# Optimization experiments

Measured on AMD Instinct MI355X. Metric: run time of the kernel, lower is better.

Reference implementation:

```python
import jax, jax.numpy as jnp
import numpy as np

B, C, N, K, COUT = 8, 128, 10000, 16, 256


def setup_inputs() -> dict:
    key = jax.random.key(0)
    ks = jax.random.split(key, 8)
    x = jax.random.normal(ks[0], (B, C, N, 1), dtype=jnp.float32)
    edge_index = jax.random.randint(ks[1], (2, B, N, K), 0, N)
    s1 = 1.0 / np.sqrt(C)
    W1 = jax.random.uniform(ks[2], (C, C), jnp.float32, -s1, s1)   # nn1 1x1 conv weight
    b1 = jax.random.uniform(ks[3], (C,), jnp.float32, -s1, s1)
    Wp = jax.random.uniform(ks[4], (C, C), jnp.float32, -s1, s1)   # nn_pooling Linear
    bp = jax.random.uniform(ks[5], (C,), jnp.float32, -s1, s1)
    s2 = 1.0 / np.sqrt(2 * C)
    W2 = jax.random.uniform(ks[6], (COUT, 2 * C), jnp.float32, -s2, s2)  # nn2 1x1 conv
    b2 = jax.random.uniform(ks[7], (COUT,), jnp.float32, -s2, s2)
    return dict(x=x, edge_index=edge_index, W1=W1, b1=b1, Wp=Wp, bp=bp, W2=W2, b2=b2)


def reference(x, edge_index, W1, b1, Wp, bp, W2, b2):
    b, c, n, _ = x.shape
    k = edge_index.shape[-1]
    # nn1: 1x1 conv (channel mix) + ReLU -> [B,C,N,1]
    h = jax.nn.relu(jnp.einsum('bcns,dc->bdns', x, W1) + b1[None, :, None, None])
    # batched_index_select: gather neighbor features along vertex dim -> [B,C,N,K]
    hn = h[:, :, :, 0]                              # [B,C,N]
    idx = edge_index[0].reshape(b, 1, n * k)        # broadcast over C
    xj = jnp.take_along_axis(hn, idx, axis=2).reshape(b, c, n, k)
    # nn_pooling: Linear over channel dim + ReLU (transpose(1,3) in torch == act on C)
    xj = jax.nn.relu(jnp.einsum('bcnk,dc->bdnk', xj, Wp) + bp[None, :, None, None])
    # max-pool over neighbors, keepdim -> [B,C,N,1]
    xj = jnp.max(xj, axis=-1, keepdims=True)
    # concat along channels, nn2: 1x1 conv + ReLU -> [B,COUT,N,1]
    cat = jnp.concatenate([h, xj], axis=1)
    out = jax.nn.relu(jnp.einsum('bcns,dc->bdns', cat, W2) + b2[None, :, None, None])
    return out
```

## Files before the change

kernel.cpp:

```cpp
#include <hip/hip_runtime.h>

#define NODES 10000
#define BATCH 8
#define CH    128
#define KNB   16
#define CO    256

typedef __bf16 bf16x8 __attribute__((ext_vector_type(8)));
typedef float  f32x4  __attribute__((ext_vector_type(4)));

__device__ __forceinline__ unsigned short f2bf(float f) {
  unsigned u = __float_as_uint(f);
  u = (u + 0x7FFFu + ((u >> 16) & 1u)) >> 16;
  return (unsigned short)u;
}

__device__ __forceinline__ unsigned pkmax(unsigned a, unsigned b) {
  unsigned d;
  asm("v_pk_max_u16 %0, %1, %2" : "=v"(d) : "v"(a), "v"(b));
  return d;
}
__device__ __forceinline__ uint4 pkmax4(uint4 a, uint4 b) {
  a.x = pkmax(a.x, b.x); a.y = pkmax(a.y, b.y);
  a.z = pkmax(a.z, b.z); a.w = pkmax(a.w, b.w);
  return a;
}
__device__ __forceinline__ bf16x8 asbf8(uint4 u) {
  union { uint4 u; bf16x8 b; } c; c.u = u; return c.b;
}

__global__ __launch_bounds__(256) void prep(
    const float* __restrict__ W1, const float* __restrict__ Wp,
    const float* __restrict__ W2,
    unsigned short* __restrict__ W1b, unsigned short* __restrict__ Wpb,
    unsigned short* __restrict__ W2b)
{
  int i = blockIdx.x * 256 + threadIdx.x;
  const float* src; unsigned short* dst; int off;
  if (i < 4096)      { src = W1; dst = W1b; off = i; }
  else if (i < 8192) { src = Wp; dst = Wpb; off = i - 4096; }
  else               { src = W2; dst = W2b; off = i - 8192; }
  float4 v = ((const float4*)src)[off];
  ushort4 o;
  o.x = f2bf(v.x); o.y = f2bf(v.y); o.z = f2bf(v.z); o.w = f2bf(v.w);
  ((ushort4*)dst)[off] = o;
}

__global__ __launch_bounds__(256) void fused_hz(
    const unsigned short* __restrict__ W1b, const float* __restrict__ b1,
    const unsigned short* __restrict__ Wpb, const float* __restrict__ bp,
    const float* __restrict__ x,
    unsigned short* __restrict__ h_t, unsigned short* __restrict__ z_t)
{
  const int b  = blockIdx.y;
  const int n0 = blockIdx.x * 64;
  const int t  = threadIdx.x;
  const int lane = t & 63, w = t >> 6;
  const int lm = lane & 15, q = lane >> 4;

  __shared__ __align__(16) unsigned short Bt[64 * 128];
  __shared__ __align__(16) unsigned short Ht[64 * 128];
  char* BtB = (char*)Bt;
  char* HtB = (char*)Ht;

  {
    const float* X = x + (size_t)b * CH * NODES;
#pragma unroll
    for (int rep = 0; rep < 4; ++rep) {
      int flat = t + rep * 256;
      int c2 = flat >> 4, n4 = flat & 15;
      int c  = c2 * 2;
      int gn = n0 + n4 * 4;
      float4 a0 = make_float4(0.f,0.f,0.f,0.f), a1 = a0;
      if (gn < NODES) {
        a0 = *(const float4*)(X + (size_t)c * NODES + gn);
        a1 = *(const float4*)(X + (size_t)(c + 1) * NODES + gn);
      }
      float v0[4] = {a0.x, a0.y, a0.z, a0.w};
      float v1[4] = {a1.x, a1.y, a1.z, a1.w};
#pragma unroll
      for (int i = 0; i < 4; ++i) {
        int nn = n4 * 4 + i;
        unsigned pk = (unsigned)f2bf(v0[i]) | ((unsigned)f2bf(v1[i]) << 16);
        int phys = nn * 256 + (((c2 >> 2) ^ (nn & 7)) << 4) + ((c2 & 3) << 2);
        *(unsigned*)(BtB + phys) = pk;
      }
    }
  }

  const int d0  = (w & 1) * 64;
  const int nbw = (w >> 1) * 32;

  uint4 af[4][4];
#pragma unroll
  for (int dt = 0; dt < 4; ++dt)
#pragma unroll
    for (int kt = 0; kt < 4; ++kt)
      af[dt][kt] = *(const uint4*)(W1b + (d0 + dt*16 + lm) * CH + kt*32 + q*8);

  __syncthreads();

  f32x4 acc[4][2];
#pragma unroll
  for (int dt = 0; dt < 4; ++dt)
#pragma unroll
    for (int nt = 0; nt < 2; ++nt) acc[dt][nt] = (f32x4){0.f,0.f,0.f,0.f};

#pragma unroll
  for (int kt = 0; kt < 4; ++kt)
#pragma unroll
    for (int nt = 0; nt < 2; ++nt) {
      int nl = nbw + nt * 16 + lm;
      int chunk = kt * 4 + q;
      int phys = nl * 256 + ((chunk ^ (nl & 7)) << 4);
      bf16x8 bb = asbf8(*(const uint4*)(BtB + phys));
#pragma unroll
      for (int dt = 0; dt < 4; ++dt)
        acc[dt][nt] = __builtin_amdgcn_mfma_f32_16x16x32_bf16(
            asbf8(af[dt][kt]), bb, acc[dt][nt], 0, 0, 0);
    }

  uint4 af2[4][4];
#pragma unroll
  for (int dt = 0; dt < 4; ++dt)
#pragma unroll
    for (int kt = 0; kt < 4; ++kt)
      af2[dt][kt] = *(const uint4*)(Wpb + (d0 + dt*16 + lm) * CH + kt*32 + q*8);

#pragma unroll
  for (int dt = 0; dt < 4; ++dt) {
    int dbase = d0 + dt * 16 + q * 4;
    float4 bi = *(const float4*)(b1 + dbase);
    float bv[4] = {bi.x, bi.y, bi.z, bi.w};
#pragma unroll
    for (int nt = 0; nt < 2; ++nt) {
      int nl = nbw + nt * 16 + lm;
      int gn = n0 + nl;
      ushort4 o;
      o.x = f2bf(fmaxf(acc[dt][nt][0] + bv[0], 0.f));
      o.y = f2bf(fmaxf(acc[dt][nt][1] + bv[1], 0.f));
      o.z = f2bf(fmaxf(acc[dt][nt][2] + bv[2], 0.f));
      o.w = f2bf(fmaxf(acc[dt][nt][3] + bv[3], 0.f));
      int chunk = dbase >> 3;
      int phys  = nl * 256 + ((chunk ^ (nl & 7)) << 4) + ((q & 1) << 3);
      *(ushort4*)(HtB + phys) = o;
      if (gn < NODES)
        *(ushort4*)(h_t + ((size_t)b * NODES + gn) * CH + dbase) = o;
    }
  }

  __syncthreads();

#pragma unroll
  for (int dt = 0; dt < 4; ++dt)
#pragma unroll
    for (int nt = 0; nt < 2; ++nt) acc[dt][nt] = (f32x4){0.f,0.f,0.f,0.f};

#pragma unroll
  for (int kt = 0; kt < 4; ++kt)
#pragma unroll
    for (int nt = 0; nt < 2; ++nt) {
      int nl = nbw + nt * 16 + lm;
      int chunk = kt * 4 + q;
      int phys = nl * 256 + ((chunk ^ (nl & 7)) << 4);
      bf16x8 bb = asbf8(*(const uint4*)(HtB + phys));
#pragma unroll
      for (int dt = 0; dt < 4; ++dt)
        acc[dt][nt] = __builtin_amdgcn_mfma_f32_16x16x32_bf16(
            asbf8(af2[dt][kt]), bb, acc[dt][nt], 0, 0, 0);
    }

#pragma unroll
  for (int dt = 0; dt < 4; ++dt) {
    int dbase = d0 + dt * 16 + q * 4;
    float4 bi = *(const float4*)(bp + dbase);
    float bv[4] = {bi.x, bi.y, bi.z, bi.w};
#pragma unroll
    for (int nt = 0; nt < 2; ++nt) {
      int gn = n0 + nbw + nt * 16 + lm;
      if (gn < NODES) {
        ushort4 o;
        o.x = f2bf(fmaxf(acc[dt][nt][0] + bv[0], 0.f));
        o.y = f2bf(fmaxf(acc[dt][nt][1] + bv[1], 0.f));
        o.z = f2bf(fmaxf(acc[dt][nt][2] + bv[2], 0.f));
        o.w = f2bf(fmaxf(acc[dt][nt][3] + bv[3], 0.f));
        *(ushort4*)(z_t + ((size_t)b * NODES + gn) * CH + dbase) = o;
      }
    }
  }
}

__global__ __launch_bounds__(256) void gmax_kernel(
    const unsigned short* __restrict__ z_t, const int* __restrict__ e0,
    unsigned short* __restrict__ zm)
{
  const int bid = blockIdx.x;
  const int b   = bid & 7;
  const int n0  = (bid >> 3) * 64;
  const int t   = threadIdx.x;
  const int nl  = t >> 2, c = t & 3;
  const int gn  = n0 + nl;
  if (gn >= NODES) return;

  const int* ip = e0 + ((size_t)b * NODES + gn) * KNB;
  int4 iv0 = *(const int4*)(ip);
  int4 iv1 = *(const int4*)(ip + 4);
  int4 iv2 = *(const int4*)(ip + 8);
  int4 iv3 = *(const int4*)(ip + 12);
  int idx[16] = {iv0.x, iv0.y, iv0.z, iv0.w,
                 iv1.x, iv1.y, iv1.z, iv1.w,
                 iv2.x, iv2.y, iv2.z, iv2.w,
                 iv3.x, iv3.y, iv3.z, iv3.w};

  const char* Z = (const char*)(z_t + (size_t)b * NODES * CH) + c * 16;
  uint4 m[4];
#pragma unroll
  for (int cg = 0; cg < 4; ++cg) m[cg] = make_uint4(0u, 0u, 0u, 0u);

#pragma unroll
  for (int k = 0; k < KNB; ++k) {
    const char* p = Z + (size_t)idx[k] * (CH * 2);
#pragma unroll
    for (int cg = 0; cg < 4; ++cg)
      m[cg] = pkmax4(m[cg], *(const uint4*)(p + cg * 64));
  }

  char* O = (char*)(zm + ((size_t)b * NODES + gn) * CH) + c * 16;
#pragma unroll
  for (int cg = 0; cg < 4; ++cg)
    *(uint4*)(O + cg * 64) = m[cg];
}

__global__ __launch_bounds__(256, 3) void out_gemm(
    const unsigned short* __restrict__ h_t, const unsigned short* __restrict__ zm,
    const unsigned short* __restrict__ W2b, const float* __restrict__ b2,
    float* __restrict__ out)
{
  const int bid = blockIdx.x;
  const int b   = bid & 7;
  const int n0  = (bid >> 3) * 64;
  const int t   = threadIdx.x;
  const int lane = t & 63, w = t >> 6;
  const int lm = lane & 15, q = lane >> 4;
  const size_t nb = (size_t)b * NODES;

  const char* hB = (const char*)h_t;
  const char* zB = (const char*)zm;

  unsigned off[4];
#pragma unroll
  for (int nt = 0; nt < 4; ++nt) {
    int gn = n0 + nt * 16 + lm;
    if (gn > NODES - 1) gn = NODES - 1;
    off[nt] = (unsigned)(((nb + (size_t)gn) * CH + q * 8) * 2);
  }

  const int d0 = w * 64;
  f32x4 acc[4][4];
#pragma unroll
  for (int dt = 0; dt < 4; ++dt)
#pragma unroll
    for (int nt = 0; nt < 4; ++nt) acc[dt][nt] = (f32x4){0.f, 0.f, 0.f, 0.f};

  uint4 acur[4], anxt[4], bcur[4], bnxt[4];
#pragma unroll
  for (int dt = 0; dt < 4; ++dt)
    acur[dt] = *(const uint4*)(W2b + (d0 + dt * 16 + lm) * CO + q * 8);
#pragma unroll
  for (int nt = 0; nt < 4; ++nt)
    bcur[nt] = *(const uint4*)(hB + off[nt]);

#pragma unroll
  for (int kt = 0; kt < 8; ++kt) {
    if (kt < 7) {
      const char* src = (kt + 1 < 4) ? hB : zB;
      int ko = ((kt + 1) & 3) * 64;
#pragma unroll
      for (int nt = 0; nt < 4; ++nt)
        bnxt[nt] = *(const uint4*)(src + off[nt] + ko);
#pragma unroll
      for (int dt = 0; dt < 4; ++dt)
        anxt[dt] = *(const uint4*)(W2b + (d0 + dt * 16 + lm) * CO
                                   + (kt + 1) * 32 + q * 8);
    }
#pragma unroll
    for (int nt = 0; nt < 4; ++nt) {
      bf16x8 bb = asbf8(bcur[nt]);
#pragma unroll
      for (int dt = 0; dt < 4; ++dt)
        acc[dt][nt] = __builtin_amdgcn_mfma_f32_16x16x32_bf16(
            asbf8(acur[dt]), bb, acc[dt][nt], 0, 0, 0);
    }
#pragma unroll
    for (int dt = 0; dt < 4; ++dt) acur[dt] = anxt[dt];
#pragma unroll
    for (int nt = 0; nt < 4; ++nt) bcur[nt] = bnxt[nt];
  }

#pragma unroll
  for (int dt = 0; dt < 4; ++dt) {
    int dbase = d0 + dt * 16 + q * 4;
    float4 bi = *(const float4*)(b2 + dbase);
    float bv[4] = {bi.x, bi.y, bi.z, bi.w};
#pragma unroll
    for (int nt = 0; nt < 4; ++nt) {
      int gn = n0 + nt * 16 + lm;
      if (gn < NODES) {
        float* op = out + ((size_t)(b * CO + dbase) * NODES) + gn;
#pragma unroll
        for (int r = 0; r < 4; ++r)
          op[(size_t)r * NODES] = fmaxf(acc[dt][nt][r] + bv[r], 0.f);
      }
    }
  }
}

extern "C" void kernel_launch(void* const* d_in, const int* in_sizes, int n_in,
                              void* d_out, int out_size, void* d_ws, size_t ws_size,
                              hipStream_t stream) {
  const float* x  = (const float*)d_in[0];
  const int*   ei = (const int*)d_in[1];
  const float* W1 = (const float*)d_in[2];
  const float* b1 = (const float*)d_in[3];
  const float* Wp = (const float*)d_in[4];
  const float* bp = (const float*)d_in[5];
  const float* W2 = (const float*)d_in[6];
  const float* b2 = (const float*)d_in[7];
  float* out = (float*)d_out;

  unsigned short* ws  = (unsigned short*)d_ws;
  unsigned short* h_t = ws;
  unsigned short* z_t = h_t + (size_t)BATCH * NODES * CH;
  unsigned short* W1b = z_t + (size_t)BATCH * NODES * CH;
  unsigned short* Wpb = W1b + CH * CH;
  unsigned short* W2b = Wpb + CH * CH;
  unsigned short* zm  = W2b + CO * 2 * CH;

  prep<<<96, 256, 0, stream>>>(W1, Wp, W2, W1b, Wpb, W2b);

  const int NT = (NODES + 63) / 64;
  fused_hz<<<dim3(NT, BATCH), 256, 0, stream>>>(W1b, b1, Wpb, bp, x, h_t, z_t);
  gmax_kernel<<<BATCH * NT, 256, 0, stream>>>(z_t, ei, zm);
  out_gemm<<<BATCH * NT, 256, 0, stream>>>(h_t, zm, W2b, b2, out);
}
```

Measured before the change: 221.5 us.

## Stage h/z stores through LDS and retile output GEMM for coalesced writes

In fused_hz, the h and z tiles are now written to swizzled shared memory first and then copied out as full 16-byte row chunks per thread, instead of scattered 8-byte stores. The z tile reuses the Bt buffer, which needs an extra barrier. out_gemm is retiled so each wave owns 16 output channels across 256 nodes, with the weight fragment held in registers for the whole K loop. Each output row is then written as contiguous node runs, improving store coalescing to the large fp32 output. The trade-offs are more accumulator registers, occupancy lowered to 2 blocks, and loss of the software prefetch double-buffering.

```diff
diff --git a/kernel.cpp b/kernel.cpp
--- a/kernel.cpp
+++ b/kernel.cpp
@@ -57,6 +57,7 @@
   const int t  = threadIdx.x;
   const int lane = t & 63, w = t >> 6;
   const int lm = lane & 15, q = lane >> 4;
+  const size_t nb = (size_t)b * NODES;
 
   __shared__ __align__(16) unsigned short Bt[64 * 128];
   __shared__ __align__(16) unsigned short Ht[64 * 128];
@@ -135,7 +136,6 @@
 #pragma unroll
     for (int nt = 0; nt < 2; ++nt) {
       int nl = nbw + nt * 16 + lm;
-      int gn = n0 + nl;
       ushort4 o;
       o.x = f2bf(fmaxf(acc[dt][nt][0] + bv[0], 0.f));
       o.y = f2bf(fmaxf(acc[dt][nt][1] + bv[1], 0.f));
@@ -144,12 +144,23 @@
       int chunk = dbase >> 3;
       int phys  = nl * 256 + ((chunk ^ (nl & 7)) << 4) + ((q & 1) << 3);
       *(ushort4*)(HtB + phys) = o;
+    }
+  }
+
+  __syncthreads();
+
+  {
+    int nl = t >> 2;
+    int gn = n0 + nl;
+#pragma unroll
+    for (int rep = 0; rep < 4; ++rep) {
+      int g = (t & 3) + rep * 4;
+      int phys = nl * 256 + ((g ^ (nl & 7)) << 4);
+      uint4 v = *(const uint4*)(HtB + phys);
       if (gn < NODES)
-        *(ushort4*)(h_t + ((size_t)b * NODES + gn) * CH + dbase) = o;
-    }
-  }
-
-  __syncthreads();
+        *(uint4*)((char*)h_t + (nb + (size_t)gn) * 256 + g * 16) = v;
+    }
+  }
 
 #pragma unroll
   for (int dt = 0; dt < 4; ++dt)
@@ -177,15 +188,30 @@
     float bv[4] = {bi.x, bi.y, bi.z, bi.w};
 #pragma unroll
     for (int nt = 0; nt < 2; ++nt) {
-      int gn = n0 + nbw + nt * 16 + lm;
-      if (gn < NODES) {
-        ushort4 o;
-        o.x = f2bf(fmaxf(acc[dt][nt][0] + bv[0], 0.f));
-        o.y = f2bf(fmaxf(acc[dt][nt][1] + bv[1], 0.f));
-        o.z = f2bf(fmaxf(acc[dt][nt][2] + bv[2], 0.f));
-        o.w = f2bf(fmaxf(acc[dt][nt][3] + bv[3], 0.f));
-        *(ushort4*)(z_t + ((size_t)b * NODES + gn) * CH + dbase) = o;
-      }
+      int nl = nbw + nt * 16 + lm;
+      ushort4 o;
+      o.x = f2bf(fmaxf(acc[dt][nt][0] + bv[0], 0.f));
+      o.y = f2bf(fmaxf(acc[dt][nt][1] + bv[1], 0.f));
+      o.z = f2bf(fmaxf(acc[dt][nt][2] + bv[2], 0.f));
+      o.w = f2bf(fmaxf(acc[dt][nt][3] + bv[3], 0.f));
+      int chunk = dbase >> 3;
+      int phys  = nl * 256 + ((chunk ^ (nl & 7)) << 4) + ((q & 1) << 3);
+      *(ushort4*)(BtB + phys) = o;
+    }
+  }
+
+  __syncthreads();
+
+  {
+    int nl = t >> 2;
+    int gn = n0 + nl;
+#pragma unroll
+    for (int rep = 0; rep < 4; ++rep) {
+      int g = (t & 3) + rep * 4;
+      int phys = nl * 256 + ((g ^ (nl & 7)) << 4);
+      uint4 v = *(const uint4*)(BtB + phys);
+      if (gn < NODES)
+        *(uint4*)((char*)z_t + (nb + (size_t)gn) * 256 + g * 16) = v;
     }
   }
 }
@@ -231,86 +257,70 @@
     *(uint4*)(O + cg * 64) = m[cg];
 }
 
-__global__ __launch_bounds__(256, 3) void out_gemm(
+__global__ __launch_bounds__(256, 2) void out_gemm(
     const unsigned short* __restrict__ h_t, const unsigned short* __restrict__ zm,
     const unsigned short* __restrict__ W2b, const float* __restrict__ b2,
     float* __restrict__ out)
 {
   const int bid = blockIdx.x;
   const int b   = bid & 7;
-  const int n0  = (bid >> 3) * 64;
+  const int r   = bid >> 3;
+  const int nr  = r >> 2;
+  const int n0  = nr * 256;
   const int t   = threadIdx.x;
   const int lane = t & 63, w = t >> 6;
+  const int d0w = (r & 3) * 64 + w * 16;
   const int lm = lane & 15, q = lane >> 4;
   const size_t nb = (size_t)b * NODES;
 
   const char* hB = (const char*)h_t;
   const char* zB = (const char*)zm;
 
-  unsigned off[4];
-#pragma unroll
-  for (int nt = 0; nt < 4; ++nt) {
+  unsigned off[16];
+#pragma unroll
+  for (int nt = 0; nt < 16; ++nt) {
     int gn = n0 + nt * 16 + lm;
     if (gn > NODES - 1) gn = NODES - 1;
     off[nt] = (unsigned)(((nb + (size_t)gn) * CH + q * 8) * 2);
   }
 
-  const int d0 = w * 64;
-  f32x4 acc[4][4];
-#pragma unroll
-  for (int dt = 0; dt < 4; ++dt)
-#pragma unroll
-    for (int nt = 0; nt < 4; ++nt) acc[dt][nt] = (f32x4){0.f, 0.f, 0.f, 0.f};
-
-  uint4 acur[4], anxt[4], bcur[4], bnxt[4];
-#pragma unroll
-  for (int dt = 0; dt < 4; ++dt)
-    acur[dt] = *(const uint4*)(W2b + (d0 + dt * 16 + lm) * CO + q * 8);
-#pragma unroll
-  for (int nt = 0; nt < 4; ++nt)
-    bcur[nt] = *(const uint4*)(hB + off[nt]);
+  uint4 af[8];
+#pragma unroll
+  for (int kt = 0; kt < 8; ++kt)
+    af[kt] = *(const uint4*)(W2b + (d0w + lm) * CO + kt * 32 + q * 8);
+
+  f32x4 acc[16];
+#pragma unroll
+  for (int nt = 0; nt < 16; ++nt) acc[nt] = (f32x4){0.f, 0.f, 0.f, 0.f};
 
 #pragma unroll
   for (int kt = 0; kt < 8; ++kt) {
-    if (kt < 7) {
-      const char* src = (kt + 1 < 4) ? hB : zB;
-      int ko = ((kt + 1) & 3) * 64;
-#pragma unroll
-      for (int nt = 0; nt < 4; ++nt)
-        bnxt[nt] = *(const uint4*)(src + off[nt] + ko);
-#pragma unroll
-      for (int dt = 0; dt < 4; ++dt)
-        anxt[dt] = *(const uint4*)(W2b + (d0 + dt * 16 + lm) * CO
-                                   + (kt + 1) * 32 + q * 8);
-    }
-#pragma unroll
-    for (int nt = 0; nt < 4; ++nt) {
-      bf16x8 bb = asbf8(bcur[nt]);
-#pragma unroll
-      for (int dt = 0; dt < 4; ++dt)
-        acc[dt][nt] = __builtin_amdgcn_mfma_f32_16x16x32_bf16(
-            asbf8(acur[dt]), bb, acc[dt][nt], 0, 0, 0);
-    }
-#pragma unroll
-    for (int dt = 0; dt < 4; ++dt) acur[dt] = anxt[dt];
-#pragma unroll
-    for (int nt = 0; nt < 4; ++nt) bcur[nt] = bnxt[nt];
-  }
-
-#pragma unroll
-  for (int dt = 0; dt < 4; ++dt) {
-    int dbase = d0 + dt * 16 + q * 4;
-    float4 bi = *(const float4*)(b2 + dbase);
-    float bv[4] = {bi.x, bi.y, bi.z, bi.w};
-#pragma unroll
-    for (int nt = 0; nt < 4; ++nt) {
+    const char* src = (kt < 4) ? hB : zB;
+    const int ko = (kt & 3) * 64;
+#pragma unroll
+    for (int hh = 0; hh < 2; ++hh) {
+      uint4 bt[8];
+#pragma unroll
+      for (int j = 0; j < 8; ++j)
+        bt[j] = *(const uint4*)(src + off[hh * 8 + j] + ko);
+#pragma unroll
+      for (int j = 0; j < 8; ++j)
+        acc[hh * 8 + j] = __builtin_amdgcn_mfma_f32_16x16x32_bf16(
+            asbf8(af[kt]), asbf8(bt[j]), acc[hh * 8 + j], 0, 0, 0);
+    }
+  }
+
+  float4 bi = *(const float4*)(b2 + d0w + q * 4);
+  float bv[4] = {bi.x, bi.y, bi.z, bi.w};
+#pragma unroll
+  for (int r4 = 0; r4 < 4; ++r4) {
+    const int d = d0w + q * 4 + r4;
+    float* op = out + (size_t)(b * CO + d) * NODES;
+#pragma unroll
+    for (int nt = 0; nt < 16; ++nt) {
       int gn = n0 + nt * 16 + lm;
-      if (gn < NODES) {
-        float* op = out + ((size_t)(b * CO + dbase) * NODES) + gn;
-#pragma unroll
-        for (int r = 0; r < 4; ++r)
-          op[(size_t)r * NODES] = fmaxf(acc[dt][nt][r] + bv[r], 0.f);
-      }
+      if (gn < NODES)
+        op[gn] = fmaxf(acc[nt][r4] + bv[r4], 0.f);
     }
   }
 }
@@ -339,7 +349,8 @@
   prep<<<96, 256, 0, stream>>>(W1, Wp, W2, W1b, Wpb, W2b);
 
   const int NT = (NODES + 63) / 64;
+  const int NR = (NODES + 255) / 256;
   fused_hz<<<dim3(NT, BATCH), 256, 0, stream>>>(W1b, b1, Wpb, bp, x, h_t, z_t);
   gmax_kernel<<<BATCH * NT, 256, 0, stream>>>(z_t, ei, zm);
-  out_gemm<<<BATCH * NT, 256, 0, stream>>>(h_t, zm, W2b, b2, out);
-}
+  out_gemm<<<BATCH * NR * 4, 256, 0, stream>>>(h_t, zm, W2b, b2, out);
+}
```

After: 267.8 us. +20.9%, slower.
